# Optimization experiments

Measured on AMD Instinct MI355X. Metric: run time of the kernel, lower is better.

## Reference

```python
import jax, jax.numpy as jnp
import numpy as np

N_NODES = 140000   # 14 frames * 10000 nodes/frame
N_EDGES = 2240000  # avg degree 16
NFEAT = 128
NHID = 128
N_FRAMES = 14


def setup_inputs() -> dict:
    key = jax.random.key(0)
    k1, k2, k3, k4, k5 = jax.random.split(key, 5)
    x = jax.random.normal(k1, (N_NODES, NFEAT), dtype=jnp.float32)
    # gc1 parameters (only layer actually used in forward)
    W = jax.random.normal(k2, (NFEAT, NHID), dtype=jnp.float32) * 0.05
    b = jnp.zeros((NHID,), dtype=jnp.float32)
    # sparse normalized adjacency as COO edge list (row sorted for fast segment_sum)
    edge_row = jnp.sort(jax.random.randint(k3, (N_EDGES,), 0, N_NODES, dtype=jnp.int32))
    edge_col = jax.random.randint(k4, (N_EDGES,), 0, N_NODES, dtype=jnp.int32)
    edge_val = jax.random.uniform(k5, (N_EDGES,), dtype=jnp.float32)
    return {"x": x, "W": W, "b": b, "edge_val": edge_val,
            "edge_row": edge_row, "edge_col": edge_col}


def reference(x, W, b, edge_val, edge_row, edge_col):
    # GraphConvolution: adj @ (x @ W) + b  (adj sparse, COO)
    support = x @ W                                   # [N, NHID]
    msgs = edge_val[:, None] * support[edge_col]      # [E, NHID] gather
    agg = jax.ops.segment_sum(msgs, edge_row, num_segments=N_NODES,
                              indices_are_sorted=True)  # [N, NHID] scatter-add
    h = jax.nn.relu(agg + b)
    # view(14, -1, c) then max over frame axis
    h = h.reshape(N_FRAMES, -1, NHID)                 # [14, N/14, NHID]
    h = jnp.max(h, axis=0)                            # [N/14, NHID]
    return jax.nn.log_softmax(h, axis=1)
```

## Files before the change

kernel.cpp:

```cpp
#include <hip/hip_runtime.h>
#include <hip/hip_bf16.h>

#define N_NODES 140000
#define N_EDGES 2240000
#define NFEAT 128
#define NHID 128
#define N_FRAMES 14
#define NODES_PER_FRAME 10000
#define CAP 352

#define N_TILES 8750
#define GEMM_GRID 512
#define WAVES_PER_BLOCK 8
#define WT_STRIDE 136
#define EDGE_BLOCKS ((N_EDGES + 255) / 256)

typedef __attribute__((ext_vector_type(8))) short frag_b16;
typedef __attribute__((ext_vector_type(4))) int frag_i4;
typedef __attribute__((ext_vector_type(4))) float f32x4;

__device__ __forceinline__ unsigned short f2bf(float f) {
    union { float f; unsigned int u; } v; v.f = f;
    unsigned int r = v.u + 0x7fffu + ((v.u >> 16) & 1u);
    return (unsigned short)(r >> 16);
}
__device__ __forceinline__ int pk_bf16(float a, float b) {
    union { __hip_bfloat162 h; int i; } u;
    u.h = __float22bfloat162_rn(make_float2(a, b));
    return u.i;
}

__global__ __launch_bounds__(256) void prep_kernel(
        const float* __restrict__ W, unsigned short* __restrict__ WT,
        const int* __restrict__ edge_row, int* __restrict__ row_ptr) {
    if (blockIdx.x < 64) {
        int e = blockIdx.x * 256 + threadIdx.x;
        int k = e >> 7, n = e & 127;
        WT[n * 128 + k] = f2bf(W[e]);
        return;
    }
    int e = (blockIdx.x - 64) * 256 + threadIdx.x;
    if (e < N_EDGES) {
        int r = edge_row[e];
        int prev = (e == 0) ? -1 : edge_row[e - 1];
        for (int q = prev + 1; q <= r; ++q) row_ptr[q] = e;
        if (e == N_EDGES - 1) {
            for (int q = r + 1; q <= N_NODES; ++q) row_ptr[q] = N_EDGES;
        }
    }
}

__global__ __launch_bounds__(512) void gemm_kernel(
        const float* __restrict__ x, const unsigned short* __restrict__ WT,
        unsigned char* __restrict__ supQ, float* __restrict__ scales) {
    __shared__ unsigned short wt_lds[128 * WT_STRIDE];

    const int wave = threadIdx.x >> 6;
    const int lane = threadIdx.x & 63;
    const int m = lane & 15;
    const int q = lane >> 4;
    const bool qb0 = (q & 1);
    const bool qb1 = (q & 2);

    int tile = blockIdx.x * WAVES_PER_BLOCK + wave;
    float4 pf[8];
    {
        const float* xr = x + (long)(tile * 16 + m) * 128 + q * 8;
#pragma unroll
        for (int ks = 0; ks < 4; ++ks) {
            pf[2 * ks]     = *(const float4*)(xr + ks * 32);
            pf[2 * ks + 1] = *(const float4*)(xr + ks * 32 + 4);
        }
    }

    const uint4* WTv = (const uint4*)WT;
    for (int idx = threadIdx.x; idx < 2048; idx += 512) {
        uint4 d = WTv[idx];
        int elem = idx << 3;
        int n = elem >> 7, k = elem & 127;
        *(uint4*)&wt_lds[n * WT_STRIDE + k] = d;
    }
    __syncthreads();

    for (;;) {
        frag_b16 xa[4];
#pragma unroll
        for (int ks = 0; ks < 4; ++ks) {
            union { frag_b16 f; frag_i4 i; } u;
            u.i[0] = pk_bf16(pf[2 * ks].x, pf[2 * ks].y);
            u.i[1] = pk_bf16(pf[2 * ks].z, pf[2 * ks].w);
            u.i[2] = pk_bf16(pf[2 * ks + 1].x, pf[2 * ks + 1].y);
            u.i[3] = pk_bf16(pf[2 * ks + 1].z, pf[2 * ks + 1].w);
            xa[ks] = u.f;
        }

        const int next = tile + GEMM_GRID * WAVES_PER_BLOCK;
        const bool more = next < N_TILES;
        if (more) {
            const float* xr = x + (long)(next * 16 + m) * 128 + q * 8;
#pragma unroll
            for (int ks = 0; ks < 4; ++ks) {
                pf[2 * ks]     = *(const float4*)(xr + ks * 32);
                pf[2 * ks + 1] = *(const float4*)(xr + ks * 32 + 4);
            }
        }

        f32x4 acc[8];
#pragma unroll
        for (int t = 0; t < 8; ++t) acc[t] = (f32x4){0.f, 0.f, 0.f, 0.f};

#pragma unroll
        for (int t = 0; t < 8; ++t) {
            const unsigned short* bp = &wt_lds[(t * 16 + m) * WT_STRIDE + q * 8];
#pragma unroll
            for (int ks = 0; ks < 4; ++ks) {
                frag_b16 wfrag = *(const frag_b16*)(bp + ks * 32);
                acc[t] = __builtin_amdgcn_mfma_f32_16x16x32_bf16(wfrag, xa[ks], acc[t], 0, 0, 0);
            }
        }

        float amax = 0.f;
#pragma unroll
        for (int t = 0; t < 8; ++t)
#pragma unroll
            for (int r = 0; r < 4; ++r) amax = fmaxf(amax, fabsf(acc[t][r]));
        amax = fmaxf(amax, __shfl_xor(amax, 16));
        amax = fmaxf(amax, __shfl_xor(amax, 32));
        float rinv = amax > 0.f ? 127.f / amax : 0.f;

        long node = (long)tile * 16 + m;
        if (q == 0) scales[node] = amax * (1.f / 127.f);

        unsigned char* srow = supQ + node * 128;
#pragma unroll
        for (int h = 0; h < 2; ++h) {
            unsigned t4[4];
#pragma unroll
            for (int t = 0; t < 4; ++t) {
                const f32x4 av = acc[4 * h + t];
                unsigned u0 = (unsigned)(rintf(av[0] * rinv) + 128.f);
                unsigned u1 = (unsigned)(rintf(av[1] * rinv) + 128.f);
                unsigned u2 = (unsigned)(rintf(av[2] * rinv) + 128.f);
                unsigned u3 = (unsigned)(rintf(av[3] * rinv) + 128.f);
                t4[t] = u0 | (u1 << 8) | (u2 << 16) | (u3 << 24);
            }
            unsigned g1 = __shfl_xor(qb0 ? t4[0] : t4[1], 16);
            unsigned g2 = __shfl_xor(qb0 ? t4[2] : t4[3], 16);
            unsigned c0 = qb0 ? g1 : t4[0];
            unsigned c1 = qb0 ? t4[1] : g1;
            unsigned c2 = qb0 ? g2 : t4[2];
            unsigned c3 = qb0 ? t4[3] : g2;
            unsigned g3 = __shfl_xor(qb1 ? c0 : c2, 32);
            unsigned g4 = __shfl_xor(qb1 ? c1 : c3, 32);
            uint4 o;
            o.x = qb1 ? g3 : c0;
            o.y = qb1 ? g4 : c1;
            o.z = qb1 ? c2 : g3;
            o.w = qb1 ? c3 : g4;
            *(uint4*)(srow + h * 64 + q * 16) = o;
        }

        if (!more) break;
        tile = next;
    }
}

__global__ __launch_bounds__(128) void agg_kernel(
        const unsigned char* __restrict__ supQ, const float* __restrict__ scales,
        const float* __restrict__ b,
        const float* __restrict__ edge_val, const int* __restrict__ edge_col,
        const int* __restrict__ row_ptr, float* __restrict__ out) {
    __shared__ int    segStart[2][8];
    __shared__ int    segLen[2][8];
    __shared__ int    segOff[2][8];
    __shared__ int2   eBuf[2][CAP];
    __shared__ float4 xch[2][32];

    const int i = blockIdx.x;
    const int lane = threadIdx.x & 63;
    const int w = threadIdx.x >> 6;
    const int eh = lane >> 5;
    const int f4 = lane & 31;
    const unsigned f4x4 = (unsigned)f4 * 4u;

    int a = 0, len = 0;
    if (lane < 7) {
        int n = (w * 7 + lane) * NODES_PER_FRAME + i;
        a = row_ptr[n];
        len = row_ptr[n + 1] - a;
    }
    int len8 = (len + 7) & ~7;
    int off = 0;
#pragma unroll
    for (int f2 = 0; f2 < 7; ++f2) {
        int L2 = __shfl(len8, f2);
        if (f2 < lane) off += L2;
    }
    if (lane < 7) { segStart[w][lane] = a; segLen[w][lane] = len; segOff[w][lane] = off; }
    if (lane == 6) segOff[w][7] = off + len8;
    __syncthreads();

    const bool fit = segOff[w][7] <= CAP;

    if (fit) {
#pragma unroll 1
        for (int f = 0; f < 7; ++f) {
            int g = segStart[w][f], s = segOff[w][f], L = segLen[w][f];
            int L8 = (L + 7) & ~7;
            for (int j = lane; j < L8; j += 64) {
                int2 v = make_int2(0, 0);
                if (j < L) {
                    int c = edge_col[g + j];
                    v.x = c;
                    v.y = __float_as_int(edge_val[g + j] * scales[c]);
                }
                eBuf[w][s + j] = v;
            }
        }
    }
    __syncthreads();

    const float4 bb = *(const float4*)&b[f4 * 4];
    float4 mx = make_float4(0.f, 0.f, 0.f, 0.f);

    if (fit) {
#pragma unroll 1
        for (int f = 0; f < 7; ++f) {
            int s = segOff[w][f];
            int e8 = s + ((segLen[w][f] + 7) & ~7);
            float a0 = 0.f, a1 = 0.f, a2 = 0.f, a3 = 0.f, svf = 0.f;
            for (int j = s; j < e8; j += 8) {
                int2 ed[4];
#pragma unroll
                for (int p = 0; p < 4; ++p) ed[p] = eBuf[w][j + 2 * p + eh];
                unsigned q4[4];
#pragma unroll
                for (int p = 0; p < 4; ++p)
                    q4[p] = *(const unsigned*)(supQ + (((unsigned)ed[p].x) << 7) + f4x4);
#pragma unroll
                for (int p = 0; p < 4; ++p) {
                    float vp = __int_as_float(ed[p].y);
                    a0 = fmaf(vp, (float)( q4[p]        & 0xffu), a0);
                    a1 = fmaf(vp, (float)((q4[p] >> 8)  & 0xffu), a1);
                    a2 = fmaf(vp, (float)((q4[p] >> 16) & 0xffu), a2);
                    a3 = fmaf(vp, (float)( q4[p] >> 24        ), a3);
                    svf += vp;
                }
            }
            a0 += __shfl_xor(a0, 32); a1 += __shfl_xor(a1, 32);
            a2 += __shfl_xor(a2, 32); a3 += __shfl_xor(a3, 32);
            svf += __shfl_xor(svf, 32);
            float h0 = fmaf(-128.f, svf, a0) + bb.x;
            float h1 = fmaf(-128.f, svf, a1) + bb.y;
            float h2 = fmaf(-128.f, svf, a2) + bb.z;
            float h3 = fmaf(-128.f, svf, a3) + bb.w;
            mx.x = fmaxf(mx.x, fmaxf(h0, 0.f));
            mx.y = fmaxf(mx.y, fmaxf(h1, 0.f));
            mx.z = fmaxf(mx.z, fmaxf(h2, 0.f));
            mx.w = fmaxf(mx.w, fmaxf(h3, 0.f));
        }
    } else {
#pragma unroll 1
        for (int f = 0; f < 7; ++f) {
            int g = segStart[w][f], L = segLen[w][f];
            float a0 = 0.f, a1 = 0.f, a2 = 0.f, a3 = 0.f, svf = 0.f;
            for (int j = eh; j < L; j += 2) {
                int c = edge_col[g + j];
                float vp = edge_val[g + j] * scales[c];
                unsigned qv = *(const unsigned*)(supQ + (((unsigned)c) << 7) + f4x4);
                a0 = fmaf(vp, (float)( qv        & 0xffu), a0);
                a1 = fmaf(vp, (float)((qv >> 8)  & 0xffu), a1);
                a2 = fmaf(vp, (float)((qv >> 16) & 0xffu), a2);
                a3 = fmaf(vp, (float)( qv >> 24        ), a3);
                svf += vp;
            }
            a0 += __shfl_xor(a0, 32); a1 += __shfl_xor(a1, 32);
            a2 += __shfl_xor(a2, 32); a3 += __shfl_xor(a3, 32);
            svf += __shfl_xor(svf, 32);
            float h0 = fmaf(-128.f, svf, a0) + bb.x;
            float h1 = fmaf(-128.f, svf, a1) + bb.y;
            float h2 = fmaf(-128.f, svf, a2) + bb.z;
            float h3 = fmaf(-128.f, svf, a3) + bb.w;
            mx.x = fmaxf(mx.x, fmaxf(h0, 0.f));
            mx.y = fmaxf(mx.y, fmaxf(h1, 0.f));
            mx.z = fmaxf(mx.z, fmaxf(h2, 0.f));
            mx.w = fmaxf(mx.w, fmaxf(h3, 0.f));
        }
    }

    if (eh == 0) xch[w][f4] = mx;
    __syncthreads();
    float4 m0 = xch[0][f4], m1 = xch[1][f4];
    float o0 = fmaxf(m0.x, m1.x);
    float o1 = fmaxf(m0.y, m1.y);
    float o2 = fmaxf(m0.z, m1.z);
    float o3 = fmaxf(m0.w, m1.w);

    float M = fmaxf(fmaxf(o0, o1), fmaxf(o2, o3));
#pragma unroll
    for (int o = 16; o >= 1; o >>= 1) M = fmaxf(M, __shfl_xor(M, o));
    float S = __expf(o0 - M) + __expf(o1 - M) + __expf(o2 - M) + __expf(o3 - M);
#pragma unroll
    for (int o = 16; o >= 1; o >>= 1) S += __shfl_xor(S, o);

    if (w == 0 && eh == 0) {
        float ls = __logf(S);
        *(float4*)&out[i * 128 + f4 * 4] =
            make_float4(o0 - M - ls, o1 - M - ls, o2 - M - ls, o3 - M - ls);
    }
}

extern "C" void kernel_launch(void* const* d_in, const int* in_sizes, int n_in,
                              void* d_out, int out_size, void* d_ws, size_t ws_size,
                              hipStream_t stream) {
    const float* x        = (const float*)d_in[0];
    const float* W        = (const float*)d_in[1];
    const float* b        = (const float*)d_in[2];
    const float* edge_val = (const float*)d_in[3];
    const int*   edge_row = (const int*)d_in[4];
    const int*   edge_col = (const int*)d_in[5];
    float* out = (float*)d_out;

    char* ws = (char*)d_ws;
    unsigned char*  supQ    = (unsigned char*)ws;
    float*          scales  = (float*)(ws + 17920000);
    unsigned short* WT      = (unsigned short*)(ws + 18480000);
    int*            row_ptr = (int*)(ws + 18512768);

    prep_kernel<<<64 + EDGE_BLOCKS, 256, 0, stream>>>(W, WT, edge_row, row_ptr);
    gemm_kernel<<<GEMM_GRID, 512, 0, stream>>>(x, WT, supQ, scales);
    agg_kernel<<<NODES_PER_FRAME, 128, 0, stream>>>(supQ, scales, b, edge_val, edge_col, row_ptr, out);
}
```

Baseline: 197.0 us.

## Flatten per-frame edge loops into one software-pipelined chunk loop

Replaces the per-frame nested loops in the aggregation kernel with a single loop over all 8-edge chunks of a wave. A per-chunk frame-id table in shared memory tells the loop when to finish one frame's reduction. Gathers for the next chunk are issued before the current chunk is accumulated, so gather latency overlaps across frame boundaries and per-frame loop overhead goes away. Empty segments get separate bias-only handling. This costs extra registers for the double-buffered data and adds a branch on each chunk.

```diff
diff --git a/kernel.cpp b/kernel.cpp
--- a/kernel.cpp
+++ b/kernel.cpp
@@ -8,6 +8,7 @@
 #define N_FRAMES 14
 #define NODES_PER_FRAME 10000
 #define CAP 352
+#define NCHUNK (CAP / 8)
 
 #define N_TILES 8750
 #define GEMM_GRID 512
@@ -174,6 +175,7 @@
     __shared__ int    segLen[2][8];
     __shared__ int    segOff[2][8];
     __shared__ int2   eBuf[2][CAP];
+    __shared__ unsigned char fidBuf[2][NCHUNK];
     __shared__ float4 xch[2][32];
 
     const int i = blockIdx.x;
@@ -198,6 +200,11 @@
     }
     if (lane < 7) { segStart[w][lane] = a; segLen[w][lane] = len; segOff[w][lane] = off; }
     if (lane == 6) segOff[w][7] = off + len8;
+    if (lane < 7) {
+        for (int c = off >> 3, ce = (off + len8) >> 3; c < ce && c < NCHUNK; ++c)
+            fidBuf[w][c] = (unsigned char)lane;
+    }
+    const bool anyEmpty = (__ballot(lane < 7 && len == 0) & 0x7full) != 0;
     __syncthreads();
 
     const bool fit = segOff[w][7] <= CAP;
@@ -224,19 +231,44 @@
     float4 mx = make_float4(0.f, 0.f, 0.f, 0.f);
 
     if (fit) {
-#pragma unroll 1
-        for (int f = 0; f < 7; ++f) {
-            int s = segOff[w][f];
-            int e8 = s + ((segLen[w][f] + 7) & ~7);
-            float a0 = 0.f, a1 = 0.f, a2 = 0.f, a3 = 0.f, svf = 0.f;
-            for (int j = s; j < e8; j += 8) {
-                int2 ed[4];
-#pragma unroll
-                for (int p = 0; p < 4; ++p) ed[p] = eBuf[w][j + 2 * p + eh];
-                unsigned q4[4];
-#pragma unroll
-                for (int p = 0; p < 4; ++p)
-                    q4[p] = *(const unsigned*)(supQ + (((unsigned)ed[p].x) << 7) + f4x4);
+        const int total = segOff[w][7];
+        float a0 = 0.f, a1 = 0.f, a2 = 0.f, a3 = 0.f, svf = 0.f;
+        if (total > 0) {
+            int curf = fidBuf[w][0];
+            int2 ed[4]; unsigned q4[4];
+#pragma unroll
+            for (int p = 0; p < 4; ++p) ed[p] = eBuf[w][2 * p + eh];
+#pragma unroll
+            for (int p = 0; p < 4; ++p)
+                q4[p] = *(const unsigned*)(supQ + (((unsigned)ed[p].x) << 7) + f4x4);
+
+            for (int j = 0; ; ) {
+                const int jn = j + 8;
+                const bool more = jn < total;
+                int2 ed2[4]; unsigned q42[4];
+                if (more) {
+#pragma unroll
+                    for (int p = 0; p < 4; ++p) ed2[p] = eBuf[w][jn + 2 * p + eh];
+#pragma unroll
+                    for (int p = 0; p < 4; ++p)
+                        q42[p] = *(const unsigned*)(supQ + (((unsigned)ed2[p].x) << 7) + f4x4);
+                }
+                const int f = fidBuf[w][j >> 3];
+                if (f != curf) {
+                    a0 += __shfl_xor(a0, 32); a1 += __shfl_xor(a1, 32);
+                    a2 += __shfl_xor(a2, 32); a3 += __shfl_xor(a3, 32);
+                    svf += __shfl_xor(svf, 32);
+                    float h0 = fmaf(-128.f, svf, a0) + bb.x;
+                    float h1 = fmaf(-128.f, svf, a1) + bb.y;
+                    float h2 = fmaf(-128.f, svf, a2) + bb.z;
+                    float h3 = fmaf(-128.f, svf, a3) + bb.w;
+                    mx.x = fmaxf(mx.x, fmaxf(h0, 0.f));
+                    mx.y = fmaxf(mx.y, fmaxf(h1, 0.f));
+                    mx.z = fmaxf(mx.z, fmaxf(h2, 0.f));
+                    mx.w = fmaxf(mx.w, fmaxf(h3, 0.f));
+                    a0 = a1 = a2 = a3 = svf = 0.f;
+                    curf = f;
+                }
 #pragma unroll
                 for (int p = 0; p < 4; ++p) {
                     float vp = __int_as_float(ed[p].y);
@@ -246,6 +278,10 @@
                     a3 = fmaf(vp, (float)( q4[p] >> 24        ), a3);
                     svf += vp;
                 }
+                if (!more) break;
+#pragma unroll
+                for (int p = 0; p < 4; ++p) { ed[p] = ed2[p]; q4[p] = q42[p]; }
+                j = jn;
             }
             a0 += __shfl_xor(a0, 32); a1 += __shfl_xor(a1, 32);
             a2 += __shfl_xor(a2, 32); a3 += __shfl_xor(a3, 32);
@@ -258,6 +294,12 @@
             mx.y = fmaxf(mx.y, fmaxf(h1, 0.f));
             mx.z = fmaxf(mx.z, fmaxf(h2, 0.f));
             mx.w = fmaxf(mx.w, fmaxf(h3, 0.f));
+        }
+        if (anyEmpty) {
+            mx.x = fmaxf(mx.x, fmaxf(bb.x, 0.f));
+            mx.y = fmaxf(mx.y, fmaxf(bb.y, 0.f));
+            mx.z = fmaxf(mx.z, fmaxf(bb.z, 0.f));
+            mx.w = fmaxf(mx.w, fmaxf(bb.w, 0.f));
         }
     } else {
 #pragma unroll 1
```

Result: no change. 197.3 us, median of 2 (+0.1%).

## Pipeline edge gathers into LDS with async global_load_lds and flat chunk loop

Applied to the files above, without the earlier changes.

Replaces the per-frame nested aggregation loop with a single flattened loop over 8-edge chunks. Each chunk carries a frame id in LDS, and accumulators are flushed whenever the frame changes. Quantized support rows are gathered asynchronously into LDS via global_load_lds, running a fixed number of chunks ahead in a ring buffer, so memory latency overlaps with the FMA work. This adds LDS usage and inline asm with hand-coded waitcnt counts, and empty frames are handled separately through a bias-only max term.

```diff
diff --git a/kernel.cpp b/kernel.cpp
--- a/kernel.cpp
+++ b/kernel.cpp
@@ -8,6 +8,8 @@
 #define N_FRAMES 14
 #define NODES_PER_FRAME 10000
 #define CAP 352
+#define NCHUNK (CAP / 8)
+#define D_PIPE 6
 
 #define N_TILES 8750
 #define GEMM_GRID 512
@@ -28,6 +30,15 @@
     union { __hip_bfloat162 h; int i; } u;
     u.h = __float22bfloat162_rn(make_float2(a, b));
     return u.i;
+}
+
+__device__ __forceinline__ unsigned lds_off(const void* p) {
+    return (unsigned)(size_t)(const __attribute__((address_space(3))) char*)p;
+}
+__device__ __forceinline__ void async_gather4(const void* g, void* l) {
+    __builtin_amdgcn_global_load_lds(
+        (const __attribute__((address_space(1))) unsigned*)g,
+        (__attribute__((address_space(3))) unsigned*)l, 4, 0, 0);
 }
 
 __global__ __launch_bounds__(256) void prep_kernel(
@@ -174,6 +185,8 @@
     __shared__ int    segLen[2][8];
     __shared__ int    segOff[2][8];
     __shared__ int2   eBuf[2][CAP];
+    __shared__ unsigned char fidBuf[2][NCHUNK];
+    __shared__ unsigned gq[2][D_PIPE][4][64];
     __shared__ float4 xch[2][32];
 
     const int i = blockIdx.x;
@@ -198,6 +211,11 @@
     }
     if (lane < 7) { segStart[w][lane] = a; segLen[w][lane] = len; segOff[w][lane] = off; }
     if (lane == 6) segOff[w][7] = off + len8;
+    if (lane < 7) {
+        for (int c = off >> 3, ce = (off + len8) >> 3; c < ce && c < NCHUNK; ++c)
+            fidBuf[w][c] = (unsigned char)lane;
+    }
+    const bool anyEmpty = (__ballot(lane < 7 && len == 0) & 0x7full) != 0;
     __syncthreads();
 
     const bool fit = segOff[w][7] <= CAP;
@@ -224,40 +242,115 @@
     float4 mx = make_float4(0.f, 0.f, 0.f, 0.f);
 
     if (fit) {
-#pragma unroll 1
-        for (int f = 0; f < 7; ++f) {
-            int s = segOff[w][f];
-            int e8 = s + ((segLen[w][f] + 7) & ~7);
-            float a0 = 0.f, a1 = 0.f, a2 = 0.f, a3 = 0.f, svf = 0.f;
-            for (int j = s; j < e8; j += 8) {
-                int2 ed[4];
-#pragma unroll
-                for (int p = 0; p < 4; ++p) ed[p] = eBuf[w][j + 2 * p + eh];
-                unsigned q4[4];
-#pragma unroll
-                for (int p = 0; p < 4; ++p)
-                    q4[p] = *(const unsigned*)(supQ + (((unsigned)ed[p].x) << 7) + f4x4);
-#pragma unroll
-                for (int p = 0; p < 4; ++p) {
-                    float vp = __int_as_float(ed[p].y);
-                    a0 = fmaf(vp, (float)( q4[p]        & 0xffu), a0);
-                    a1 = fmaf(vp, (float)((q4[p] >> 8)  & 0xffu), a1);
-                    a2 = fmaf(vp, (float)((q4[p] >> 16) & 0xffu), a2);
-                    a3 = fmaf(vp, (float)( q4[p] >> 24        ), a3);
-                    svf += vp;
-                }
-            }
-            a0 += __shfl_xor(a0, 32); a1 += __shfl_xor(a1, 32);
-            a2 += __shfl_xor(a2, 32); a3 += __shfl_xor(a3, 32);
-            svf += __shfl_xor(svf, 32);
-            float h0 = fmaf(-128.f, svf, a0) + bb.x;
-            float h1 = fmaf(-128.f, svf, a1) + bb.y;
-            float h2 = fmaf(-128.f, svf, a2) + bb.z;
-            float h3 = fmaf(-128.f, svf, a3) + bb.w;
-            mx.x = fmaxf(mx.x, fmaxf(h0, 0.f));
-            mx.y = fmaxf(mx.y, fmaxf(h1, 0.f));
-            mx.z = fmaxf(mx.z, fmaxf(h2, 0.f));
-            mx.w = fmaxf(mx.w, fmaxf(h3, 0.f));
+        const int total = segOff[w][7];
+        float a0 = 0.f, a1 = 0.f, a2 = 0.f, a3 = 0.f, svf = 0.f;
+        if (total > 0) {
+            const int nch = total >> 3;
+            const unsigned ebW  = lds_off(&eBuf[w][0]) + (unsigned)eh * 8u;
+            const unsigned gqW  = lds_off(&gq[w][0][0][0]) + (unsigned)lane * 4u;
+            const unsigned fidW = lds_off(&fidBuf[w][0]);
+            int curf = fidBuf[w][0];
+
+            auto FLUSH = [&]() {
+                a0 += __shfl_xor(a0, 32); a1 += __shfl_xor(a1, 32);
+                a2 += __shfl_xor(a2, 32); a3 += __shfl_xor(a3, 32);
+                svf += __shfl_xor(svf, 32);
+                float h0 = fmaf(-128.f, svf, a0) + bb.x;
+                float h1 = fmaf(-128.f, svf, a1) + bb.y;
+                float h2 = fmaf(-128.f, svf, a2) + bb.z;
+                float h3 = fmaf(-128.f, svf, a3) + bb.w;
+                mx.x = fmaxf(mx.x, fmaxf(h0, 0.f));
+                mx.y = fmaxf(mx.y, fmaxf(h1, 0.f));
+                mx.z = fmaxf(mx.z, fmaxf(h2, 0.f));
+                mx.w = fmaxf(mx.w, fmaxf(h3, 0.f));
+                a0 = a1 = a2 = a3 = svf = 0.f;
+            };
+
+            auto ISSUE = [&](unsigned ea, int sl) {
+                unsigned c0, c1, c2, c3;
+                asm volatile(
+                    "ds_read_b32 %0, %4\n\t"
+                    "ds_read_b32 %1, %4 offset:16\n\t"
+                    "ds_read_b32 %2, %4 offset:32\n\t"
+                    "ds_read_b32 %3, %4 offset:48\n\t"
+                    "s_waitcnt lgkmcnt(0)"
+                    : "=&v"(c0), "=&v"(c1), "=&v"(c2), "=&v"(c3)
+                    : "v"(ea) : "memory");
+                async_gather4(supQ + (((size_t)c0) << 7) + f4x4, &gq[w][sl][0][0]);
+                async_gather4(supQ + (((size_t)c1) << 7) + f4x4, &gq[w][sl][1][0]);
+                async_gather4(supQ + (((size_t)c2) << 7) + f4x4, &gq[w][sl][2][0]);
+                async_gather4(supQ + (((size_t)c3) << 7) + f4x4, &gq[w][sl][3][0]);
+            };
+
+            auto CONSUME = [&](unsigned qa, unsigned va, unsigned fa) {
+                unsigned q0, q1, q2, q3, v0, v1, v2, v3, fv;
+                asm volatile(
+                    "ds_read_u8 %8, %11\n\t"
+                    "ds_read_b32 %0, %9\n\t"
+                    "ds_read_b32 %1, %9 offset:256\n\t"
+                    "ds_read_b32 %2, %9 offset:512\n\t"
+                    "ds_read_b32 %3, %9 offset:768\n\t"
+                    "ds_read_b32 %4, %10\n\t"
+                    "ds_read_b32 %5, %10 offset:16\n\t"
+                    "ds_read_b32 %6, %10 offset:32\n\t"
+                    "ds_read_b32 %7, %10 offset:48\n\t"
+                    "s_waitcnt lgkmcnt(0)"
+                    : "=&v"(q0), "=&v"(q1), "=&v"(q2), "=&v"(q3),
+                      "=&v"(v0), "=&v"(v1), "=&v"(v2), "=&v"(v3), "=&v"(fv)
+                    : "v"(qa), "v"(va), "v"(fa) : "memory");
+                if ((int)fv != curf) { FLUSH(); curf = (int)fv; }
+                float p0 = __int_as_float(v0);
+                a0 = fmaf(p0, (float)( q0        & 0xffu), a0);
+                a1 = fmaf(p0, (float)((q0 >> 8)  & 0xffu), a1);
+                a2 = fmaf(p0, (float)((q0 >> 16) & 0xffu), a2);
+                a3 = fmaf(p0, (float)( q0 >> 24        ), a3);
+                svf += p0;
+                float p1 = __int_as_float(v1);
+                a0 = fmaf(p1, (float)( q1        & 0xffu), a0);
+                a1 = fmaf(p1, (float)((q1 >> 8)  & 0xffu), a1);
+                a2 = fmaf(p1, (float)((q1 >> 16) & 0xffu), a2);
+                a3 = fmaf(p1, (float)( q1 >> 24        ), a3);
+                svf += p1;
+                float p2 = __int_as_float(v2);
+                a0 = fmaf(p2, (float)( q2        & 0xffu), a0);
+                a1 = fmaf(p2, (float)((q2 >> 8)  & 0xffu), a1);
+                a2 = fmaf(p2, (float)((q2 >> 16) & 0xffu), a2);
+                a3 = fmaf(p2, (float)( q2 >> 24        ), a3);
+                svf += p2;
+                float p3 = __int_as_float(v3);
+                a0 = fmaf(p3, (float)( q3        & 0xffu), a0);
+                a1 = fmaf(p3, (float)((q3 >> 8)  & 0xffu), a1);
+                a2 = fmaf(p3, (float)((q3 >> 16) & 0xffu), a2);
+                a3 = fmaf(p3, (float)( q3 >> 24        ), a3);
+                svf += p3;
+            };
+
+            unsigned eaddr = ebW;
+            const int npro = nch < D_PIPE ? nch : D_PIPE;
+            for (int c = 0; c < npro; ++c) { ISSUE(eaddr, c); eaddr += 64u; }
+
+            int slot = 0, j = 0;
+            unsigned va = ebW + 4u, fa = fidW;
+            for (; j < nch - D_PIPE; ++j) {
+                asm volatile("s_waitcnt vmcnt(20)" ::: "memory");
+                CONSUME(gqW + ((unsigned)slot << 10), va, fa);
+                ISSUE(eaddr, slot);
+                eaddr += 64u; va += 64u; fa += 1u;
+                slot = (slot == D_PIPE - 1) ? 0 : slot + 1;
+            }
+            asm volatile("s_waitcnt vmcnt(0)" ::: "memory");
+            for (; j < nch; ++j) {
+                CONSUME(gqW + ((unsigned)slot << 10), va, fa);
+                va += 64u; fa += 1u;
+                slot = (slot == D_PIPE - 1) ? 0 : slot + 1;
+            }
+            FLUSH();
+        }
+        if (anyEmpty) {
+            mx.x = fmaxf(mx.x, fmaxf(bb.x, 0.f));
+            mx.y = fmaxf(mx.y, fmaxf(bb.y, 0.f));
+            mx.z = fmaxf(mx.z, fmaxf(bb.z, 0.f));
+            mx.w = fmaxf(mx.w, fmaxf(bb.w, 0.f));
         }
     } else {
 #pragma unroll 1
```

New measurement: 218.9 us. 1.11x slower.
